# Kernel tuning notes

Measured on AMD Instinct MI355X. Metric: run time of the kernel, lower is better.

## Reference

```python
import jax, jax.numpy as jnp
import numpy as np

B, T, D = 2, 2048, 1024
N_HEADS, N_KV_HEADS = 16, 4
D_HEAD = D // N_HEADS            # 64
N_GROUPS = N_HEADS // N_KV_HEADS  # 4
ROPE_THETA = 10000.0


def _rope_freqs(t, d_head, theta):
    inv = 1.0 / (theta ** (jnp.arange(0, d_head, 2, dtype=jnp.float32) / d_head))  # (d_head/2,)
    ang = jnp.arange(t, dtype=jnp.float32)[:, None] * inv[None, :]                 # (T, d_head/2)
    return jnp.stack([jnp.cos(ang), jnp.sin(ang)], axis=-1)                        # (T, d_head/2, 2)


def _apply_rope(x, freqs):
    # x: (B, T, H, d_head); freqs: (T, d_head/2, 2) = (cos, sin)
    xr = x.reshape(*x.shape[:-1], -1, 2)          # (B,T,H,d/2,2)
    xre, xim = xr[..., 0], xr[..., 1]
    fre = freqs[None, :, None, :, 0]              # (1,T,1,d/2)
    fim = freqs[None, :, None, :, 1]
    outre = xre * fre - xim * fim
    outim = xre * fim + xim * fre
    return jnp.stack([outre, outim], axis=-1).reshape(x.shape)


def setup_inputs() -> dict:
    key = jax.random.key(0)
    ks = jax.random.split(key, 5)
    x = jax.random.normal(ks[0], (B, T, D), dtype=jnp.float32)
    w_q = jax.random.normal(ks[1], (N_HEADS * D_HEAD, D), dtype=jnp.float32) * 0.02
    w_k = jax.random.normal(ks[2], (N_KV_HEADS * D_HEAD, D), dtype=jnp.float32) * 0.02
    w_v = jax.random.normal(ks[3], (N_KV_HEADS * D_HEAD, D), dtype=jnp.float32) * 0.02
    w_o = jax.random.normal(ks[4], (D, N_HEADS * D_HEAD), dtype=jnp.float32) * 0.02
    rope_freqs = _rope_freqs(T, D_HEAD, ROPE_THETA)
    causal = jnp.tril(jnp.ones((T, T), dtype=bool))
    mask = jnp.where(causal, 0.0, -1e9).astype(jnp.float32)[None, None]  # (1,1,T,T)
    return {"x": x, "rope_freqs": rope_freqs, "mask": mask,
            "w_q": w_q, "w_k": w_k, "w_v": w_v, "w_o": w_o}


def reference(x, rope_freqs, mask, w_q, w_k, w_v, w_o):
    # projections (torch Linear: y = x @ W.T)
    q = jnp.einsum('btd,od->bto', x, w_q).reshape(B, T, N_HEADS, D_HEAD)
    k = jnp.einsum('btd,od->bto', x, w_k).reshape(B, T, N_KV_HEADS, D_HEAD)
    v = jnp.einsum('btd,od->bto', x, w_v).reshape(B, T, N_KV_HEADS, D_HEAD)
    q = _apply_rope(q, rope_freqs)
    k = _apply_rope(k, rope_freqs)
    # GQA: expand KV heads (kv head h -> N_GROUPS contiguous query heads)
    k = jnp.repeat(k, N_GROUPS, axis=2)   # (B,T,H,d)
    v = jnp.repeat(v, N_GROUPS, axis=2)
    q = q.transpose(0, 2, 1, 3)           # (B,H,T,d)
    k = k.transpose(0, 2, 1, 3)
    v = v.transpose(0, 2, 1, 3)
    scale = 1.0 / np.sqrt(D_HEAD).astype(np.float32)
    scores = jnp.einsum('bhqd,bhkd->bhqk', q, k) * scale + mask
    attn = jax.nn.softmax(scores, axis=-1)
    out = jnp.einsum('bhqk,bhkd->bhqd', attn, v)
    out = out.transpose(0, 2, 1, 3).reshape(B, T, N_HEADS * D_HEAD)
    return jnp.einsum('bto,do->btd', out, w_o)
```

## Files before the change

### kernel.cpp

```cpp
#include <hip/hip_runtime.h>
#include <hip/hip_bf16.h>
#include <cstddef>
#include <type_traits>

#define TT   2048
#define NH   16
#define NKV  4
#define DH   64

typedef __bf16 bf16x8 __attribute__((ext_vector_type(8)));
typedef float  f32x4  __attribute__((ext_vector_type(4)));

#if __has_builtin(__builtin_amdgcn_exp2f)
#define EXP2F(x) __builtin_amdgcn_exp2f(x)
#else
#define EXP2F(x) __expf((x) * 0.69314718056f)
#endif

#define QSCALE 0.180336880f

__global__ __launch_bounds__(256)
void cast_kernel(const float* __restrict__ x,  const float* __restrict__ wq,
                 const float* __restrict__ wk, const float* __restrict__ wv,
                 const float* __restrict__ wo,
                 __bf16* __restrict__ xb, __bf16* __restrict__ wqkv,
                 __bf16* __restrict__ wob)
{
    const int g = blockIdx.x * 256 + threadIdx.x;
    const float* src;
    __bf16* dst;
    int off;
    if (g < 1048576)       { src = x;  dst = xb;   off = g; }
    else if (g < 1310720)  { src = wq; dst = wqkv; off = g - 1048576; }
    else if (g < 1376256)  { src = wk; dst = wqkv + 1048576; off = g - 1310720; }
    else if (g < 1441792)  { src = wv; dst = wqkv + 1310720; off = g - 1376256; }
    else                   { src = wo; dst = wob;  off = g - 1441792; }
    const float4 v = *(const float4*)(src + (size_t)off * 4);
    union { __bf16 h[4]; uint2 u; } o;
    o.h[0] = (__bf16)v.x; o.h[1] = (__bf16)v.y;
    o.h[2] = (__bf16)v.z; o.h[3] = (__bf16)v.w;
    *(uint2*)(dst + (size_t)off * 4) = o.u;
}

template<int MODE>
__global__ __launch_bounds__(256, 3)
void mm_kernel(const __bf16* __restrict__ A,
               const __bf16* __restrict__ W,
               const float* __restrict__ rope,
               void* __restrict__ O0, void* __restrict__ O1,
               void* __restrict__ O2)
{
    constexpr int K  = 1024;
    constexpr int NK = K / 32;
    constexpr int NX = (MODE == 0) ? 12 : 8;
    __shared__ __bf16 As[2][64 * 32];
    __shared__ __bf16 Bs[2][128 * 32];

    const int tid  = threadIdx.x;
    const int lane = tid & 63;
    const int wv   = tid >> 6;
    const int quad = lane >> 4;
    const int lc   = lane & 15;

    const int dlin = blockIdx.x + NX * blockIdx.y;
    const int nid  = (dlin & 7) * ((NX * 64) >> 3) + (dlin >> 3);
    const int bx   = nid % NX;
    const int by   = nid / NX;

    const int gm0  = by * 64;
    const int gn0  = bx * 128;
    const int wc0  = wv * 32;

    size_t gaA;  int lsA;
    {
        const int p = tid;
        const int r = p >> 2, q = (p & 3) ^ ((r >> 1) & 3);
        gaA = (size_t)r * K + q * 8;
        lsA = p * 8;
    }
    size_t gaB[2]; int lsB[2];
#pragma unroll
    for (int j = 0; j < 2; j++) {
        const int p = tid + j * 256;
        const int r = p >> 2, q = (p & 3) ^ ((r >> 1) & 3);
        gaB[j] = (size_t)r * K + q * 8;
        lsB[j] = p * 8;
    }
    const __bf16* Ag = A + (size_t)gm0 * K;
    const __bf16* Wg = W + (size_t)gn0 * K;

    auto foff = [&](int row) { return (row * 4 + (quad ^ ((row >> 1) & 3))) * 8; };
    int aoff[4], boff[2];
#pragma unroll
    for (int i = 0; i < 4; i++) aoff[i] = foff(i * 16 + lc);
#pragma unroll
    for (int j = 0; j < 2; j++) boff[j] = foff(wc0 + j * 16 + lc);

    f32x4 acc[4][2];
#pragma unroll
    for (int i = 0; i < 4; i++)
#pragma unroll
        for (int j = 0; j < 2; j++) acc[i][j] = (f32x4){0.f, 0.f, 0.f, 0.f};

    bf16x8 ar[2], br[2][2];

    ar[0] = *(const bf16x8*)(Ag + gaA);
#pragma unroll
    for (int j = 0; j < 2; j++) br[0][j] = *(const bf16x8*)(Wg + gaB[j]);
    *(bf16x8*)&As[0][lsA] = ar[0];
#pragma unroll
    for (int j = 0; j < 2; j++) *(bf16x8*)&Bs[0][lsB[j]] = br[0][j];
    ar[1] = *(const bf16x8*)(Ag + gaA + 32);
#pragma unroll
    for (int j = 0; j < 2; j++) br[1][j] = *(const bf16x8*)(Wg + gaB[j] + 32);
    ar[0] = *(const bf16x8*)(Ag + gaA + 64);
#pragma unroll
    for (int j = 0; j < 2; j++) br[0][j] = *(const bf16x8*)(Wg + gaB[j] + 64);
    __syncthreads();

    auto step = [&](int kt, auto pc) {
        constexpr int P = decltype(pc)::value;
        constexpr int Q = 1 - P;
        bf16x8 af[4], bfr[2];
#pragma unroll
        for (int i = 0; i < 4; i++) af[i]  = *(const bf16x8*)&As[P][aoff[i]];
#pragma unroll
        for (int j = 0; j < 2; j++) bfr[j] = *(const bf16x8*)&Bs[P][boff[j]];
        if (kt + 1 < NK) {
            *(bf16x8*)&As[Q][lsA] = ar[Q];
#pragma unroll
            for (int j = 0; j < 2; j++) *(bf16x8*)&Bs[Q][lsB[j]] = br[Q][j];
        }
#pragma unroll
        for (int i = 0; i < 4; i++)
#pragma unroll
            for (int j = 0; j < 2; j++)
                acc[i][j] = __builtin_amdgcn_mfma_f32_16x16x32_bf16(
                    af[i], bfr[j], acc[i][j], 0, 0, 0);
        if (kt + 3 < NK) {
            const int kb = (kt + 3) * 32;
            ar[Q] = *(const bf16x8*)(Ag + gaA + kb);
#pragma unroll
            for (int j = 0; j < 2; j++) br[Q][j] = *(const bf16x8*)(Wg + gaB[j] + kb);
        }
        if (kt + 1 < NK) __syncthreads();
    };
    for (int kt = 0; kt < NK; kt += 2) {
        step(kt,     std::integral_constant<int, 0>{});
        step(kt + 1, std::integral_constant<int, 1>{});
    }

    if (MODE == 0) {
        __bf16* Qo = (__bf16*)O0;
        __bf16* Ko = (__bf16*)O1;
        __bf16* Vo = (__bf16*)O2;
        const int region = (gn0 < 1024) ? 0 : (gn0 < 1280) ? 1 : 2;
#pragma unroll
        for (int i = 0; i < 4; i++) {
#pragma unroll
            for (int r = 0; r < 4; r++) {
                const int grow = gm0 + i * 16 + quad * 4 + r;
                const int b = grow >> 11, t = grow & 2047;
                const float* rrow = rope + t * 64;
#pragma unroll
                for (int j = 0; j < 2; j++) {
                    const float v = acc[i][j][r];
                    const float partner = __shfl_xor(v, 1, 64);
                    const int col = gn0 + wc0 + j * 16 + lc;
                    if (region == 0) {
                        const int h = col >> 6, d = col & 63;
                        const float2 cs = *(const float2*)(rrow + (d >> 1) * 2);
                        const float out = v * cs.x + partner * ((d & 1) ? cs.y : -cs.y);
                        Qo[((size_t)(b * NH + h) * TT + t) * DH + d] = (__bf16)(out * QSCALE);
                    } else if (region == 1) {
                        const int ck = col - 1024;
                        const int kh = ck >> 6, d = ck & 63;
                        const float2 cs = *(const float2*)(rrow + (d >> 1) * 2);
                        const float out = v * cs.x + partner * ((d & 1) ? cs.y : -cs.y);
                        Ko[((size_t)(b * NKV + kh) * TT + t) * DH + d] = (__bf16)out;
                    } else {
                        const int cv = col - 1280;
                        const int kh = cv >> 6, d = cv & 63;
                        Vo[((size_t)(b * NKV + kh) * DH + d) * TT + t] = (__bf16)v;
                    }
                }
            }
        }
    } else {
        float* Of = (float*)O0;
#pragma unroll
        for (int i = 0; i < 4; i++)
#pragma unroll
            for (int r = 0; r < 4; r++) {
                const int grow = gm0 + i * 16 + quad * 4 + r;
#pragma unroll
                for (int j = 0; j < 2; j++)
                    Of[(size_t)grow * 1024 + gn0 + wc0 + j * 16 + lc] = acc[i][j][r];
            }
    }
}

__global__ __launch_bounds__(256, 4)
void attn_kernel(const __bf16* __restrict__ Q,
                 const __bf16* __restrict__ K,
                 const __bf16* __restrict__ Vt,
                 __bf16* __restrict__ O)
{
    __shared__ __bf16 Ks[64 * 64];
    __shared__ __bf16 Vs[64 * 64];
    __shared__ __bf16 Ps[4][16][72];

    const int tid  = threadIdx.x;
    const int lane = tid & 63;
    const int wv   = tid >> 6;
    const int quad = lane >> 4;
    const int lc   = lane & 15;

    const int a   = blockIdx.x & 31;
    const int rep = blockIdx.x >> 5;
    const int qt  = ((rep >> 3) & 1) ? (31 - a) : a;
    const int b   = rep >> 4;
    const int h   = rep & 15;
    const int kh  = h >> 2;
    const int nk  = qt + 1;

    const __bf16* Kg = K  + (size_t)(b * NKV + kh) * TT * DH;
    const __bf16* Vg = Vt + (size_t)(b * NKV + kh) * DH * TT;

    bf16x8 qb[2];
    {
        const __bf16* qp = Q + ((size_t)(b * NH + h) * TT
                                + qt * 64 + wv * 16 + lc) * DH;
        qb[0] = *(const bf16x8*)(qp + quad * 8);
        qb[1] = *(const bf16x8*)(qp + 32 + quad * 8);
    }

    int koff[2], voff[2], lsl[2];
#pragma unroll
    for (int j = 0; j < 2; j++) {
        const int p  = tid + j * 256;
        const int r  = p >> 3;
        const int qs = (p & 7) ^ (r & 7);
        koff[j] = r * DH + qs * 8;
        voff[j] = r * TT + qs * 8;
        lsl[j]  = p * 8;
    }

    int foff[4][2];
#pragma unroll
    for (int g = 0; g < 4; g++)
#pragma unroll
        for (int c = 0; c < 2; c++)
            foff[g][c] = ((g * 16 + lc) * 8 + ((c * 4 + quad) ^ (lc & 7))) * 8;

    float l_s = 0.f;
    f32x4 oacc[4];
#pragma unroll
    for (int g = 0; g < 4; g++) oacc[g] = (f32x4){0.f, 0.f, 0.f, 0.f};

    bf16x8 kr[2], vr[2];
    auto load_regs = [&](int kt) {
        const __bf16* kp = Kg + (size_t)kt * 64 * DH;
        const __bf16* vp = Vg + (size_t)kt * 64;
#pragma unroll
        for (int j = 0; j < 2; j++) {
            kr[j] = *(const bf16x8*)(kp + koff[j]);
            vr[j] = *(const bf16x8*)(vp + voff[j]);
        }
    };
    auto store_lds = [&]() {
#pragma unroll
        for (int j = 0; j < 2; j++) {
            *(bf16x8*)&Ks[lsl[j]] = kr[j];
            *(bf16x8*)&Vs[lsl[j]] = vr[j];
        }
    };

    load_regs(0);
    store_lds();
    if (nk > 1) load_regs(1);
    __syncthreads();

    for (int kt = 0; kt < nk; kt++) {
        bf16x8 ka[4][2];
#pragma unroll
        for (int g = 0; g < 4; g++) {
            ka[g][0] = *(const bf16x8*)&Ks[foff[g][0]];
            ka[g][1] = *(const bf16x8*)&Ks[foff[g][1]];
        }

        const int D = qt * 64 + wv * 16 - kt * 64;

        f32x4 s[4];
        __builtin_amdgcn_s_setprio(1);
#pragma unroll
        for (int g = 0; g < 4; g++) {
            f32x4 z = (f32x4){0.f, 0.f, 0.f, 0.f};
            z = __builtin_amdgcn_mfma_f32_16x16x32_bf16(ka[g][0], qb[0], z, 0, 0, 0);
            z = __builtin_amdgcn_mfma_f32_16x16x32_bf16(ka[g][1], qb[1], z, 0, 0, 0);
            s[g] = z;
        }
        __builtin_amdgcn_s_setprio(0);

        if (D < 63) {
            const int thr = D + lc;
#pragma unroll
            for (int g = 0; g < 4; g++)
#pragma unroll
                for (int r = 0; r < 4; r++)
                    if (g * 16 + quad * 4 + r > thr) s[g][r] = -1e30f;
        }

        float rs = 0.f;
#pragma unroll
        for (int g = 0; g < 4; g++) {
#pragma unroll
            for (int r = 0; r < 4; r++) {
                s[g][r] = EXP2F(s[g][r]);
                rs += s[g][r];
            }
            union { __bf16 hh[4]; uint2 uu; } pk;
            pk.hh[0] = (__bf16)s[g][0]; pk.hh[1] = (__bf16)s[g][1];
            pk.hh[2] = (__bf16)s[g][2]; pk.hh[3] = (__bf16)s[g][3];
            *(uint2*)&Ps[wv][lc][g * 16 + quad * 4] = pk.uu;
        }
        l_s += rs;

        bf16x8 va[4][2];
#pragma unroll
        for (int g = 0; g < 4; g++) {
            va[g][0] = *(const bf16x8*)&Vs[foff[g][0]];
            va[g][1] = *(const bf16x8*)&Vs[foff[g][1]];
        }

        const bf16x8 pb0 = *(const bf16x8*)&Ps[wv][lc][quad * 8];
        const bf16x8 pb1 = *(const bf16x8*)&Ps[wv][lc][32 + quad * 8];
        __builtin_amdgcn_s_setprio(1);
#pragma unroll
        for (int g = 0; g < 4; g++) {
            oacc[g] = __builtin_amdgcn_mfma_f32_16x16x32_bf16(va[g][0], pb0, oacc[g], 0, 0, 0);
            oacc[g] = __builtin_amdgcn_mfma_f32_16x16x32_bf16(va[g][1], pb1, oacc[g], 0, 0, 0);
        }
        __builtin_amdgcn_s_setprio(0);

        if (kt + 1 < nk) {
            __syncthreads();
            store_lds();
            if (kt + 2 < nk) load_regs(kt + 2);
            __syncthreads();
        }
    }

    {
        float l = l_s;
        l += __shfl_xor(l, 16, 64);
        l += __shfl_xor(l, 32, 64);
        const float inv = 1.f / l;
        const int t = qt * 64 + wv * 16 + lc;
        __bf16* op = O + (size_t)(b * TT + t) * (NH * DH) + h * DH;
#pragma unroll
        for (int g = 0; g < 4; g++) {
            union { __bf16 hh[4]; uint2 uu; } pk;
            pk.hh[0] = (__bf16)(oacc[g][0] * inv);
            pk.hh[1] = (__bf16)(oacc[g][1] * inv);
            pk.hh[2] = (__bf16)(oacc[g][2] * inv);
            pk.hh[3] = (__bf16)(oacc[g][3] * inv);
            *(uint2*)(op + g * 16 + quad * 4) = pk.uu;
        }
    }
}

extern "C" void kernel_launch(void* const* d_in, const int* in_sizes, int n_in,
                              void* d_out, int out_size, void* d_ws, size_t ws_size,
                              hipStream_t stream)
{
    const float* x    = (const float*)d_in[0];
    const float* rope = (const float*)d_in[1];
    const float* w_q  = (const float*)d_in[3];
    const float* w_k  = (const float*)d_in[4];
    const float* w_v  = (const float*)d_in[5];
    const float* w_o  = (const float*)d_in[6];
    float* out = (float*)d_out;

    char* ws = (char*)d_ws;
    __bf16* Qb   = (__bf16*)(ws);
    __bf16* Kb   = (__bf16*)(ws + (8  << 20));
    __bf16* Vtb  = (__bf16*)(ws + (10 << 20));
    __bf16* AOb  = (__bf16*)(ws + (12 << 20));
    __bf16* xb   = (__bf16*)(ws + (20 << 20));
    __bf16* Wqkv = (__bf16*)(ws + (28 << 20));
    __bf16* Wob  = (__bf16*)(ws + (31 << 20));

    cast_kernel<<<6656, dim3(256), 0, stream>>>(x, w_q, w_k, w_v, w_o,
                                                xb, Wqkv, Wob);

    dim3 g1(12, 64);
    mm_kernel<0><<<g1, dim3(256), 0, stream>>>(xb, Wqkv, rope,
                                               (void*)Qb, (void*)Kb, (void*)Vtb);

    attn_kernel<<<1024, dim3(256), 0, stream>>>(Qb, Kb, Vtb, AOb);

    dim3 g3(8, 64);
    mm_kernel<1><<<g3, dim3(256), 0, stream>>>(AOb, Wob, rope,
                                               (void*)out, nullptr, nullptr);
}
```

Baseline: 176.7 us.

## Double-buffer K/V tiles in LDS and swizzle the P scratch layout

The attention kernel now keeps two LDS buffers for K and V tiles. The next tile is written into the alternate buffer right after the current K fragments are read, which removes one of the two barriers per iteration. The P scratch drops its padding and uses an XOR swizzle to avoid bank conflicts. LDS use roughly doubles, which may lower occupancy under the 4-blocks-per-CU launch bound. The early store also depends on register-loaded data arriving in time.

```diff
diff --git a/kernel.cpp b/kernel.cpp
--- a/kernel.cpp
+++ b/kernel.cpp
@@ -206,9 +206,9 @@
                  const __bf16* __restrict__ Vt,
                  __bf16* __restrict__ O)
 {
-    __shared__ __bf16 Ks[64 * 64];
-    __shared__ __bf16 Vs[64 * 64];
-    __shared__ __bf16 Ps[4][16][72];
+    __shared__ __bf16 Ks[2][64 * 64];
+    __shared__ __bf16 Vs[2][64 * 64];
+    __shared__ __bf16 Ps[4][16][64];
 
     const int tid  = threadIdx.x;
     const int lane = tid & 63;
@@ -253,6 +253,9 @@
         for (int c = 0; c < 2; c++)
             foff[g][c] = ((g * 16 + lc) * 8 + ((c * 4 + quad) ^ (lc & 7))) * 8;
 
+    const int psw = 2 * (lc & 7);
+    char* prow = (char*)&Ps[wv][lc][0];
+
     float l_s = 0.f;
     f32x4 oacc[4];
 #pragma unroll
@@ -268,26 +271,30 @@
             vr[j] = *(const bf16x8*)(vp + voff[j]);
         }
     };
-    auto store_lds = [&]() {
+    auto store_lds = [&](int buf) {
 #pragma unroll
         for (int j = 0; j < 2; j++) {
-            *(bf16x8*)&Ks[lsl[j]] = kr[j];
-            *(bf16x8*)&Vs[lsl[j]] = vr[j];
+            *(bf16x8*)&Ks[buf][lsl[j]] = kr[j];
+            *(bf16x8*)&Vs[buf][lsl[j]] = vr[j];
         }
     };
 
     load_regs(0);
-    store_lds();
+    store_lds(0);
     if (nk > 1) load_regs(1);
     __syncthreads();
 
     for (int kt = 0; kt < nk; kt++) {
+        const int cur = kt & 1;
+
         bf16x8 ka[4][2];
 #pragma unroll
         for (int g = 0; g < 4; g++) {
-            ka[g][0] = *(const bf16x8*)&Ks[foff[g][0]];
-            ka[g][1] = *(const bf16x8*)&Ks[foff[g][1]];
-        }
+            ka[g][0] = *(const bf16x8*)&Ks[cur][foff[g][0]];
+            ka[g][1] = *(const bf16x8*)&Ks[cur][foff[g][1]];
+        }
+
+        if (kt + 1 < nk) store_lds(cur ^ 1);
 
         const int D = qt * 64 + wv * 16 - kt * 64;
 
@@ -322,19 +329,19 @@
             union { __bf16 hh[4]; uint2 uu; } pk;
             pk.hh[0] = (__bf16)s[g][0]; pk.hh[1] = (__bf16)s[g][1];
             pk.hh[2] = (__bf16)s[g][2]; pk.hh[3] = (__bf16)s[g][3];
-            *(uint2*)&Ps[wv][lc][g * 16 + quad * 4] = pk.uu;
+            *(uint2*)(prow + ((4 * g + quad) ^ psw) * 8) = pk.uu;
         }
         l_s += rs;
 
         bf16x8 va[4][2];
 #pragma unroll
         for (int g = 0; g < 4; g++) {
-            va[g][0] = *(const bf16x8*)&Vs[foff[g][0]];
-            va[g][1] = *(const bf16x8*)&Vs[foff[g][1]];
-        }
-
-        const bf16x8 pb0 = *(const bf16x8*)&Ps[wv][lc][quad * 8];
-        const bf16x8 pb1 = *(const bf16x8*)&Ps[wv][lc][32 + quad * 8];
+            va[g][0] = *(const bf16x8*)&Vs[cur][foff[g][0]];
+            va[g][1] = *(const bf16x8*)&Vs[cur][foff[g][1]];
+        }
+
+        const bf16x8 pb0 = *(const bf16x8*)(prow + (( 2 * quad) ^ psw) * 8);
+        const bf16x8 pb1 = *(const bf16x8*)(prow + ((8 + 2 * quad) ^ psw) * 8);
         __builtin_amdgcn_s_setprio(1);
 #pragma unroll
         for (int g = 0; g < 4; g++) {
@@ -343,12 +350,8 @@
         }
         __builtin_amdgcn_s_setprio(0);
 
-        if (kt + 1 < nk) {
-            __syncthreads();
-            store_lds();
-            if (kt + 2 < nk) load_regs(kt + 2);
-            __syncthreads();
-        }
+        if (kt + 2 < nk) load_regs(kt + 2);
+        if (kt + 1 < nk) __syncthreads();
     }
 
     {
```

Measured after the change: 169.3 us (median of 2 runs). 1.04x faster.
